# Optimization experiments

Hardware: AMD Instinct MI355X
Metric: run time of the kernel (lower is better)

Reference implementation:

```python
import jax, jax.numpy as jnp
import numpy as np

B, F, T, N, A, E_INC, NUM_EDGES, C_OUT = 32, 64, 20, 512, 64, 2048, 128, 128
C_IN = F + A


def setup_inputs() -> dict:
    key = jax.random.key(0)
    k = jax.random.split(key, 6)
    x = jax.random.normal(k[0], (B, F, T, N), dtype=jnp.float32)
    H = jax.random.randint(k[1], (B, T, 2, E_INC), 0, NUM_EDGES)  # row0: node ids, row1: hyperedge ids
    ssa = jax.random.normal(k[2], (B, T, N, A), dtype=jnp.float32)
    W = jax.random.uniform(k[3], (B, T, E_INC), dtype=jnp.float32)  # unused by conv (matches original)
    theta = jax.random.normal(k[4], (C_OUT, C_IN), dtype=jnp.float32) / np.sqrt(C_IN).astype(np.float32)
    bias = jnp.zeros((C_OUT,), dtype=jnp.float32)
    return {"x": x, "H": H, "ssa": ssa, "W": W, "theta": theta, "bias": bias}


def _hconv(feat, hidx, theta, bias):
    # One PyG HypergraphConv (no attention, unit hyperedge weights):
    #   out = D^{-1} H B^{-1} H^T (X Theta^T) + b
    # feat: [N, C_in], hidx: [2, E_inc]
    node_idx, edge_idx = hidx[0], hidx[1]
    xp = feat @ theta.T  # [N, C_out]
    ones = jnp.ones(node_idx.shape, dtype=xp.dtype)
    deg_n = jax.ops.segment_sum(ones, node_idx, num_segments=N)         # D
    deg_e = jax.ops.segment_sum(ones, edge_idx, num_segments=NUM_EDGES)  # B
    Dinv = jnp.where(deg_n > 0, 1.0 / deg_n, 0.0)
    Binv = jnp.where(deg_e > 0, 1.0 / deg_e, 0.0)
    # node -> hyperedge aggregation
    edge_feat = Binv[:, None] * jax.ops.segment_sum(xp[node_idx], edge_idx, num_segments=NUM_EDGES)
    # hyperedge -> node aggregation
    out = Dinv[:, None] * jax.ops.segment_sum(edge_feat[edge_idx], node_idx, num_segments=N)
    return out + bias


def reference(x, H, ssa, W, theta, bias):
    # x: [B, F, T, N] -> [B, T, N, F], concat scene attention -> [B, T, N, C_in]
    feat = jnp.concatenate([jnp.transpose(x, (0, 2, 3, 1)), ssa], axis=-1)
    conv = lambda f, h: _hconv(f, h, theta, bias)
    out = jax.vmap(jax.vmap(conv))(feat, H)  # [B, T, N, C_out]
    # Original does a raw .reshape(B, C_out, T, N) (NOT a permute) -- replicate exactly.
    return out.reshape(B, C_OUT, T, N)
```

## Files before the change

kernel.cpp:

```cpp
#include <hip/hip_runtime.h>
#include <cstdint>
#include <cstddef>

namespace {

constexpr int B_ = 32, F_ = 64, T_ = 20, N_ = 512, A_ = 64;
constexpr int EINC = 2048, NEDGE = 128, COUT = 128, CIN = 128;
constexpr int THREADS = 1024;

constexpr int L_SRT  = 0;
constexpr int L_ESRT = 2048;
constexpr int L_OFFN = 4096;
constexpr int L_OFFE = 4612;
constexpr int L_DEGN = 4744;
constexpr int L_DEGE = 5256;
constexpr int L_CURN = 5384;
constexpr int L_CURE = 5896;
constexpr int L_U    = 6024;
constexpr int L_ST   = 14472;
constexpr int LDS_WORDS = 19592;
constexpr int LDS_BYTES = LDS_WORDS * 4;
constexpr int XQ_STRIDE = 66;

typedef float f32x8 __attribute__((ext_vector_type(8)));
typedef float f32x4v __attribute__((ext_vector_type(4)));
typedef short bf16x8v __attribute__((ext_vector_type(8)));

__device__ inline unsigned short f2bf(float f) {
    unsigned int u = __float_as_uint(f);
    u = u + 0x7FFFu + ((u >> 16) & 1u);
    return (unsigned short)(u >> 16);
}
__device__ inline unsigned packbf(float lo, float hi) {
    return ((unsigned)f2bf(hi) << 16) | (unsigned)f2bf(lo);
}

#define LOAD_CHUNK(CC, DST) do {                                              \
    const int c_ = (CC);                                                      \
    if (c_ < 4) {                                                             \
        const float* xr_ = x + (((size_t)b * F_ + (c_ * 16 + hf * 8)) * T_ + t) * N_ + n; \
        _Pragma("unroll")                                                     \
        for (int j_ = 0; j_ < 8; ++j_)                                        \
            DST[j_] = xr_[(size_t)j_ * T_ * N_];                              \
    } else {                                                                  \
        const float* sr_ = ssa + ((size_t)bt * N_ + n) * A_ + (c_ - 4) * 16 + hf * 8; \
        float4 u0_ = *(const float4*)(sr_);                                   \
        float4 u1_ = *(const float4*)(sr_ + 4);                               \
        DST[0] = u0_.x; DST[1] = u0_.y; DST[2] = u0_.z; DST[3] = u0_.w;       \
        DST[4] = u1_.x; DST[5] = u1_.y; DST[6] = u1_.z; DST[7] = u1_.w;       \
    }                                                                         \
} while (0)

#define P6PASS(P) do {                                                        \
    const int lw_ = tid & 31;                                                 \
    const int g_  = tid >> 5;                                                 \
    float2 bsv_ = *(const float2*)(bias + (P) * 64 + 2 * lw_);                \
    for (int nn_ = g_; nn_ < N_; nn_ += 32) {                                 \
        int o0_ = s_ofn[nn_], o1_ = s_ofn[nn_ + 1];                           \
        float f0_ = 0.f, f1_ = 0.f;                                           \
        for (int k_ = o0_; k_ < o1_; ++k_) {                                  \
            int e_ = s_srt[k_];                                               \
            float2 xv_ = *(const float2*)(s_xq + e_ * XQ_STRIDE + 2 * lw_);   \
            f0_ += xv_.x; f1_ += xv_.y;                                       \
        }                                                                     \
        float dinv_ = (o1_ > o0_) ? 1.0f / (float)(o1_ - o0_) : 0.0f;         \
        size_t ob_ = ((size_t)bt * N_ + nn_) * COUT + (P) * 64 + 2 * lw_;     \
        *(float2*)(out + ob_) = make_float2(f0_ * dinv_ + bsv_.x,             \
                                            f1_ * dinv_ + bsv_.y);            \
    }                                                                         \
} while (0)

__global__ __launch_bounds__(256)
void theta_pack(const float* __restrict__ theta, unsigned* __restrict__ ws) {
    int w = blockIdx.x * 256 + threadIdx.x;
    int f = w >> 8, rem = w & 255;
    int l = rem >> 2, kq = rem & 3;
    int kk = f & 3, cti = (f >> 2) & 3, ch2 = f >> 4;
    int co = ch2 * 64 + cti * 16 + (l & 15);
    int ci = kk * 32 + (l >> 4) * 8 + kq * 2;
    const float2 tv = *(const float2*)(theta + (size_t)co * CIN + ci);
    ws[w] = packbf(tv.x, tv.y);
}

__global__ __launch_bounds__(THREADS, 8)
void hgconv(const float* __restrict__ x, const int* __restrict__ H,
            const float* __restrict__ ssa, const float* __restrict__ theta,
            const float* __restrict__ bias, float* __restrict__ out,
            const unsigned* __restrict__ thw)
{
    extern __shared__ float sf[];
    int* si = (int*)sf;

    const int tid = (int)threadIdx.x;
    const int bt  = (int)blockIdx.x;
    const int b   = bt / T_;
    const int t   = bt - b * T_;

    int* s_srt = si + L_SRT;
    int* s_esr = si + L_ESRT;
    int* s_ofn = si + L_OFFN;
    int* s_ofe = si + L_OFFE;
    int* s_dgn = si + L_DEGN;
    int* s_dge = si + L_DEGE;
    int* s_cun = si + L_CURN;
    int* s_cue = si + L_CURE;
    int* s_nid = si + L_U;
    int* s_eid = si + L_U + EINC;
    unsigned* s_eq16 = (unsigned*)si + L_U;
    float* s_xq = sf + L_U;
    unsigned* s_st16 = (unsigned*)si + L_ST;

    const int n  = tid & (N_ - 1);
    const int hf = tid >> 9;

    const int* Hb = H + (size_t)bt * (2 * EINC);
    #pragma unroll
    for (int k = 0; k < EINC / THREADS; ++k) {
        int i = tid + k * THREADS;
        s_nid[i] = Hb[i];
        s_eid[i] = Hb[EINC + i];
    }
    if (tid < N_)    s_dgn[tid] = 0;
    if (tid < NEDGE) s_dge[tid] = 0;
    __syncthreads();

    #pragma unroll
    for (int k = 0; k < EINC / THREADS; ++k) {
        int i = tid + k * THREADS;
        atomicAdd(&s_dgn[s_nid[i]], 1);
        atomicAdd(&s_dge[s_eid[i]], 1);
    }
    __syncthreads();

    const bool act = s_dgn[n] > 0;
    f32x8 vv;
    if (act) LOAD_CHUNK(0, vv);

    if (tid < 64) {
        const int l = tid;
        int d0 = s_dge[2 * l], d1 = s_dge[2 * l + 1];
        int run = d0 + d1;
        int scan = run;
        #pragma unroll
        for (int d = 1; d < 64; d <<= 1) {
            int o = __shfl_up(scan, d);
            if (l >= d) scan += o;
        }
        int excl = scan - run;
        s_ofe[2 * l] = excl;
        s_ofe[2 * l + 1] = excl + d0;
        if (l == 63) s_ofe[NEDGE] = scan;
    } else if (tid < 128) {
        const int l = tid & 63;
        int v, loc[8], run = 0;
        #pragma unroll
        for (int q = 0; q < 8; ++q) { v = s_dgn[l * 8 + q]; loc[q] = run; run += v; }
        int scan = run;
        #pragma unroll
        for (int d = 1; d < 64; d <<= 1) {
            int o = __shfl_up(scan, d);
            if (l >= d) scan += o;
        }
        int excl = scan - run;
        #pragma unroll
        for (int q = 0; q < 8; ++q) s_ofn[l * 8 + q] = excl + loc[q];
        if (l == 63) s_ofn[N_] = scan;
    }
    __syncthreads();

    if (tid < N_)    s_cun[tid] = s_ofn[tid];
    if (tid < NEDGE) s_cue[tid] = s_ofe[tid];
    __syncthreads();

    #pragma unroll
    for (int k = 0; k < EINC / THREADS; ++k) {
        int i = tid + k * THREADS;
        int nd = s_nid[i];
        int e  = s_eid[i];
        int pe = atomicAdd(&s_cue[e], 1);
        s_esr[pe] = nd;
        int pn = atomicAdd(&s_cun[nd], 1);
        s_srt[pn] = e;
    }
    __syncthreads();

    const int eg = tid >> 3;
    const int ep = tid & 7;
    for (int c = 0; c < 8; ++c) {
        if (act) {
            unsigned w0 = packbf(vv[0], vv[1]), w1 = packbf(vv[2], vv[3]);
            unsigned w2 = packbf(vv[4], vv[5]), w3 = packbf(vv[6], vv[7]);
            unsigned* sp = s_st16 + n * 10 + hf * 4;
            *(uint2*)(sp)     = make_uint2(w0, w1);
            *(uint2*)(sp + 2) = make_uint2(w2, w3);
        }
        __syncthreads();

        f32x8 nv;
        if (c < 7 && act) LOAD_CHUNK(c + 1, nv);

        {
            int k0 = s_ofe[eg], k1 = s_ofe[eg + 1];
            float a0 = 0.f, a1 = 0.f;
            int k = k0;
            for (; k + 1 < k1; k += 2) {
                unsigned pA = s_st16[s_esr[k] * 10 + ep];
                unsigned pB = s_st16[s_esr[k + 1] * 10 + ep];
                a0 += __uint_as_float(pA << 16) + __uint_as_float(pB << 16);
                a1 += __uint_as_float(pA & 0xFFFF0000u) + __uint_as_float(pB & 0xFFFF0000u);
            }
            if (k < k1) {
                unsigned pA = s_st16[s_esr[k] * 10 + ep];
                a0 += __uint_as_float(pA << 16);
                a1 += __uint_as_float(pA & 0xFFFF0000u);
            }
            float binv = (k1 > k0) ? 1.0f / (float)(k1 - k0) : 0.0f;
            int p = c * 8 + ep;
            s_eq16[eg * 64 + (p ^ ((eg & 7) << 2))] = packbf(a0 * binv, a1 * binv);
        }
        __syncthreads();

        if (c < 7 && act) vv = nv;
    }

    {
        const int wv = tid >> 6, l = tid & 63;
        const int rt = wv >> 1, ch2 = wv & 1;
        const int r  = rt * 16 + (l & 15);
        const int q  = l >> 4;
        const int lco = l & 15;

        bf16x8v av[4];
        #pragma unroll
        for (int kk = 0; kk < 4; ++kk) {
            int aw = r * 64 + ((kk * 16 + q * 4) ^ ((r & 7) << 2));
            av[kk] = *(const bf16x8v*)(s_eq16 + aw);
        }
        f32x4v acc[4];
        #pragma unroll
        for (int i = 0; i < 4; ++i) acc[i] = (f32x4v){0.f, 0.f, 0.f, 0.f};

        if (thw) {
            #pragma unroll
            for (int cti = 0; cti < 4; ++cti) {
                #pragma unroll
                for (int kk = 0; kk < 4; ++kk) {
                    int f = (ch2 * 4 + cti) * 4 + kk;
                    uint4 u = *((const uint4*)thw + f * 64 + l);
                    bf16x8v bv = *(const bf16x8v*)&u;
                    acc[cti] = __builtin_amdgcn_mfma_f32_16x16x32_bf16(av[kk], bv, acc[cti], 0, 0, 0);
                }
            }
        } else {
            #pragma unroll
            for (int cti = 0; cti < 4; ++cti) {
                const int co = ch2 * 64 + cti * 16 + lco;
                #pragma unroll
                for (int kk = 0; kk < 4; ++kk) {
                    const float* tp = theta + (size_t)co * CIN + kk * 32 + q * 8;
                    float4 t0 = *(const float4*)tp;
                    float4 t1 = *(const float4*)(tp + 4);
                    unsigned pw[4] = { packbf(t0.x, t0.y), packbf(t0.z, t0.w),
                                       packbf(t1.x, t1.y), packbf(t1.z, t1.w) };
                    bf16x8v bv = *(const bf16x8v*)pw;
                    acc[cti] = __builtin_amdgcn_mfma_f32_16x16x32_bf16(av[kk], bv, acc[cti], 0, 0, 0);
                }
            }
        }
        __syncthreads();

        if (ch2 == 0) {
            #pragma unroll
            for (int cti = 0; cti < 4; ++cti)
                #pragma unroll
                for (int reg = 0; reg < 4; ++reg)
                    s_xq[(rt * 16 + q * 4 + reg) * XQ_STRIDE + cti * 16 + lco] = acc[cti][reg];
        }
        __syncthreads();
        P6PASS(0);
        __syncthreads();
        if (ch2 == 1) {
            #pragma unroll
            for (int cti = 0; cti < 4; ++cti)
                #pragma unroll
                for (int reg = 0; reg < 4; ++reg)
                    s_xq[(rt * 16 + q * 4 + reg) * XQ_STRIDE + cti * 16 + lco] = acc[cti][reg];
        }
        __syncthreads();
        P6PASS(1);
    }
}

}

extern "C" void kernel_launch(void* const* d_in, const int* in_sizes, int n_in,
                              void* d_out, int out_size, void* d_ws, size_t ws_size,
                              hipStream_t stream) {
    const float* x     = (const float*)d_in[0];
    const int*   H     = (const int*)d_in[1];
    const float* ssa   = (const float*)d_in[2];
    const float* theta = (const float*)d_in[4];
    const float* bias  = (const float*)d_in[5];
    float* outp = (float*)d_out;

    const bool use_ws = (d_ws != nullptr) && (ws_size >= 32768);
    if (use_ws)
        hipLaunchKernelGGL(theta_pack, dim3(32), dim3(256), 0, stream,
                           theta, (unsigned*)d_ws);

    (void)hipFuncSetAttribute((const void*)&hgconv,
                              hipFuncAttributeMaxDynamicSharedMemorySize, LDS_BYTES);

    hipLaunchKernelGGL(hgconv, dim3(B_ * T_), dim3(THREADS), LDS_BYTES, stream,
                       x, H, ssa, theta, bias, outp,
                       use_ws ? (const unsigned*)d_ws : nullptr);
}
```

Before: 91.95 us.

## Halve block size, compact LDS indices, interleave MFMA with edge aggregation

The block shrinks from 1024 to 512 threads, each handling one node and 16 channels per chunk. Sorted index arrays are stored as bytes and shorts instead of ints, and a XOR swizzle replaces the padded LDS layout. This cuts LDS use from about 78KB to about 38KB so more blocks can be resident per CU. The theta GEMM is now issued incrementally: after every two channel chunks, each wave runs MFMAs for one K-slice across all 8 output tiles, keeping 8 accumulators live. The cost is higher register pressure and more per-thread gather work in the aggregation loops.

```diff
diff --git a/kernel.cpp b/kernel.cpp
--- a/kernel.cpp
+++ b/kernel.cpp
@@ -6,23 +6,22 @@
 
 constexpr int B_ = 32, F_ = 64, T_ = 20, N_ = 512, A_ = 64;
 constexpr int EINC = 2048, NEDGE = 128, COUT = 128, CIN = 128;
-constexpr int THREADS = 1024;
-
-constexpr int L_SRT  = 0;
-constexpr int L_ESRT = 2048;
-constexpr int L_OFFN = 4096;
-constexpr int L_OFFE = 4612;
-constexpr int L_DEGN = 4744;
-constexpr int L_DEGE = 5256;
-constexpr int L_CURN = 5384;
-constexpr int L_CURE = 5896;
-constexpr int L_U    = 6024;
-constexpr int L_ST   = 14472;
-constexpr int LDS_WORDS = 19592;
+constexpr int THREADS = 512;
+
+constexpr int L_SRT8 = 0;
+constexpr int L_OFN  = 512;
+constexpr int L_OFE  = 1028;
+constexpr int L_DGE  = 1160;
+constexpr int L_CUE  = 1288;
+constexpr int L_DGN  = 1416;
+constexpr int L_CUN  = 1928;
+constexpr int L_ESR  = 2440;
+constexpr int L_EQ   = 3464;
+constexpr int L_ST   = 5512;
+constexpr int LDS_WORDS = 9608;
 constexpr int LDS_BYTES = LDS_WORDS * 4;
-constexpr int XQ_STRIDE = 66;
-
-typedef float f32x8 __attribute__((ext_vector_type(8)));
+
+typedef unsigned u32x8 __attribute__((ext_vector_type(8)));
 typedef float f32x4v __attribute__((ext_vector_type(4)));
 typedef short bf16x8v __attribute__((ext_vector_type(8)));
 
@@ -34,33 +33,40 @@
 __device__ inline unsigned packbf(float lo, float hi) {
     return ((unsigned)f2bf(hi) << 16) | (unsigned)f2bf(lo);
 }
+__device__ inline float bflo(unsigned p) { return __uint_as_float(p << 16); }
+__device__ inline float bfhi(unsigned p) { return __uint_as_float(p & 0xFFFF0000u); }
 
 #define LOAD_CHUNK(CC, DST) do {                                              \
     const int c_ = (CC);                                                      \
     if (c_ < 4) {                                                             \
-        const float* xr_ = x + (((size_t)b * F_ + (c_ * 16 + hf * 8)) * T_ + t) * N_ + n; \
+        const float* xr_ = x + (((size_t)b * F_ + c_ * 16) * T_ + t) * N_ + n; \
         _Pragma("unroll")                                                     \
-        for (int j_ = 0; j_ < 8; ++j_)                                        \
-            DST[j_] = xr_[(size_t)j_ * T_ * N_];                              \
+        for (int m_ = 0; m_ < 8; ++m_) {                                      \
+            float f0_ = xr_[(size_t)(2 * m_) * (T_ * N_)];                    \
+            float f1_ = xr_[(size_t)(2 * m_ + 1) * (T_ * N_)];                \
+            DST[m_] = packbf(f0_, f1_);                                       \
+        }                                                                     \
     } else {                                                                  \
-        const float* sr_ = ssa + ((size_t)bt * N_ + n) * A_ + (c_ - 4) * 16 + hf * 8; \
-        float4 u0_ = *(const float4*)(sr_);                                   \
-        float4 u1_ = *(const float4*)(sr_ + 4);                               \
-        DST[0] = u0_.x; DST[1] = u0_.y; DST[2] = u0_.z; DST[3] = u0_.w;       \
-        DST[4] = u1_.x; DST[5] = u1_.y; DST[6] = u1_.z; DST[7] = u1_.w;       \
+        const float* sr_ = ssa + ((size_t)bt * N_ + n) * A_ + (c_ - 4) * 16;  \
+        _Pragma("unroll")                                                     \
+        for (int m_ = 0; m_ < 4; ++m_) {                                      \
+            float4 u_ = *(const float4*)(sr_ + 4 * m_);                       \
+            DST[2 * m_]     = packbf(u_.x, u_.y);                             \
+            DST[2 * m_ + 1] = packbf(u_.z, u_.w);                             \
+        }                                                                     \
     }                                                                         \
 } while (0)
 
 #define P6PASS(P) do {                                                        \
     const int lw_ = tid & 31;                                                 \
-    const int g_  = tid >> 5;                                                 \
+    const int g_  = tid >> 5;                                      \
     float2 bsv_ = *(const float2*)(bias + (P) * 64 + 2 * lw_);                \
-    for (int nn_ = g_; nn_ < N_; nn_ += 32) {                                 \
+    for (int nn_ = g_; nn_ < N_; nn_ += 16) {                                 \
         int o0_ = s_ofn[nn_], o1_ = s_ofn[nn_ + 1];                           \
         float f0_ = 0.f, f1_ = 0.f;                                           \
         for (int k_ = o0_; k_ < o1_; ++k_) {                                  \
-            int e_ = s_srt[k_];                                               \
-            float2 xv_ = *(const float2*)(s_xq + e_ * XQ_STRIDE + 2 * lw_);   \
+            int e_ = (int)s_srt8[k_];                                         \
+            float2 xv_ = *(const float2*)(s_xq + e_ * 64 + 2 * lw_);          \
             f0_ += xv_.x; f1_ += xv_.y;                                       \
         }                                                                     \
         float dinv_ = (o1_ > o0_) ? 1.0f / (float)(o1_ - o0_) : 0.0f;         \
@@ -75,8 +81,8 @@
     int w = blockIdx.x * 256 + threadIdx.x;
     int f = w >> 8, rem = w & 255;
     int l = rem >> 2, kq = rem & 3;
-    int kk = f & 3, cti = (f >> 2) & 3, ch2 = f >> 4;
-    int co = ch2 * 64 + cti * 16 + (l & 15);
+    int kk = f & 3, ct = f >> 2;
+    int co = ct * 16 + (l & 15);
     int ci = kk * 32 + (l >> 4) * 8 + kq * 2;
     const float2 tv = *(const float2*)(theta + (size_t)co * CIN + ci);
     ws[w] = packbf(tv.x, tv.y);
@@ -96,22 +102,21 @@
     const int b   = bt / T_;
     const int t   = bt - b * T_;
 
-    int* s_srt = si + L_SRT;
-    int* s_esr = si + L_ESRT;
-    int* s_ofn = si + L_OFFN;
-    int* s_ofe = si + L_OFFE;
-    int* s_dgn = si + L_DEGN;
-    int* s_dge = si + L_DEGE;
-    int* s_cun = si + L_CURN;
-    int* s_cue = si + L_CURE;
-    int* s_nid = si + L_U;
-    int* s_eid = si + L_U + EINC;
-    unsigned* s_eq16 = (unsigned*)si + L_U;
-    float* s_xq = sf + L_U;
-    unsigned* s_st16 = (unsigned*)si + L_ST;
-
-    const int n  = tid & (N_ - 1);
-    const int hf = tid >> 9;
+    unsigned char*  s_srt8  = (unsigned char*)(si + L_SRT8);
+    int*            s_ofn   = si + L_OFN;
+    int*            s_ofe   = si + L_OFE;
+    int*            s_dge   = si + L_DGE;
+    int*            s_cue   = si + L_CUE;
+    int*            s_dgn   = si + L_DGN;
+    int*            s_cun   = si + L_CUN;
+    unsigned short* s_esr16 = (unsigned short*)(si + L_ESR);
+    unsigned*       s_eq16  = (unsigned*)(si + L_EQ);
+    unsigned*       s_st16  = (unsigned*)(si + L_ST);
+    int*            s_nid   = si + L_EQ;
+    int*            s_eid   = si + L_EQ + EINC;
+    float*          s_xq    = sf + L_DGN;
+
+    const int n = tid;
 
     const int* Hb = H + (size_t)bt * (2 * EINC);
     #pragma unroll
@@ -120,7 +125,7 @@
         s_nid[i] = Hb[i];
         s_eid[i] = Hb[EINC + i];
     }
-    if (tid < N_)    s_dgn[tid] = 0;
+    s_dgn[tid] = 0;
     if (tid < NEDGE) s_dge[tid] = 0;
     __syncthreads();
 
@@ -133,7 +138,7 @@
     __syncthreads();
 
     const bool act = s_dgn[n] > 0;
-    f32x8 vv;
+    u32x8 vv;
     if (act) LOAD_CHUNK(0, vv);
 
     if (tid < 64) {
@@ -168,7 +173,7 @@
     }
     __syncthreads();
 
-    if (tid < N_)    s_cun[tid] = s_ofn[tid];
+    s_cun[tid] = s_ofn[tid];
     if (tid < NEDGE) s_cue[tid] = s_ofe[tid];
     __syncthreads();
 
@@ -178,117 +183,97 @@
         int nd = s_nid[i];
         int e  = s_eid[i];
         int pe = atomicAdd(&s_cue[e], 1);
-        s_esr[pe] = nd;
+        s_esr16[pe] = (unsigned short)nd;
         int pn = atomicAdd(&s_cun[nd], 1);
-        s_srt[pn] = e;
-    }
-    __syncthreads();
-
-    const int eg = tid >> 3;
-    const int ep = tid & 7;
+        s_srt8[pn] = (unsigned char)e;
+    }
+    __syncthreads();
+
+    const int eg = tid >> 2;
+    const int ep = tid & 3;
+    const int wv = tid >> 6, l = tid & 63;
+    const int q  = l >> 4, lco = l & 15;
+    const int r  = wv * 16 + lco;
+    const int aoff = r * 16 + 4 * (q ^ (r & 3) ^ ((r >> 2) & 3));
+    const int k0 = s_ofe[eg], k1 = s_ofe[eg + 1];
+    const float binv = (k1 > k0) ? 1.0f / (float)(k1 - k0) : 0.0f;
+
+    f32x4v acc[8];
+    #pragma unroll
+    for (int i = 0; i < 8; ++i) acc[i] = (f32x4v){0.f, 0.f, 0.f, 0.f};
+
     for (int c = 0; c < 8; ++c) {
         if (act) {
-            unsigned w0 = packbf(vv[0], vv[1]), w1 = packbf(vv[2], vv[3]);
-            unsigned w2 = packbf(vv[4], vv[5]), w3 = packbf(vv[6], vv[7]);
-            unsigned* sp = s_st16 + n * 10 + hf * 4;
-            *(uint2*)(sp)     = make_uint2(w0, w1);
-            *(uint2*)(sp + 2) = make_uint2(w2, w3);
+            #pragma unroll
+            for (int p2 = 0; p2 < 4; ++p2) {
+                unsigned* sp = s_st16 + n * 8
+                             + 2 * (p2 ^ (n & 3) ^ ((n >> 2) & 3));
+                *(uint2*)sp = make_uint2(vv[2 * p2], vv[2 * p2 + 1]);
+            }
         }
         __syncthreads();
 
-        f32x8 nv;
+        u32x8 nv;
         if (c < 7 && act) LOAD_CHUNK(c + 1, nv);
 
         {
-            int k0 = s_ofe[eg], k1 = s_ofe[eg + 1];
-            float a0 = 0.f, a1 = 0.f;
-            int k = k0;
-            for (; k + 1 < k1; k += 2) {
-                unsigned pA = s_st16[s_esr[k] * 10 + ep];
-                unsigned pB = s_st16[s_esr[k + 1] * 10 + ep];
-                a0 += __uint_as_float(pA << 16) + __uint_as_float(pB << 16);
-                a1 += __uint_as_float(pA & 0xFFFF0000u) + __uint_as_float(pB & 0xFFFF0000u);
+            float a0 = 0.f, a1 = 0.f, a2 = 0.f, a3 = 0.f;
+            for (int k = k0; k < k1; ++k) {
+                int nd = (int)s_esr16[k];
+                uint2 pr = *(const uint2*)(s_st16 + nd * 8
+                                + 2 * (ep ^ (nd & 3) ^ ((nd >> 2) & 3)));
+                a0 += bflo(pr.x); a1 += bfhi(pr.x);
+                a2 += bflo(pr.y); a3 += bfhi(pr.y);
             }
-            if (k < k1) {
-                unsigned pA = s_st16[s_esr[k] * 10 + ep];
-                a0 += __uint_as_float(pA << 16);
-                a1 += __uint_as_float(pA & 0xFFFF0000u);
-            }
-            float binv = (k1 > k0) ? 1.0f / (float)(k1 - k0) : 0.0f;
-            int p = c * 8 + ep;
-            s_eq16[eg * 64 + (p ^ ((eg & 7) << 2))] = packbf(a0 * binv, a1 * binv);
+            int slot = (((c & 1) * 2 + (ep >> 1)) ^ (eg & 3) ^ ((eg >> 2) & 3));
+            *(uint2*)(s_eq16 + eg * 16 + 4 * slot + (ep & 1) * 2) =
+                make_uint2(packbf(a0 * binv, a1 * binv), packbf(a2 * binv, a3 * binv));
         }
         __syncthreads();
 
-        if (c < 7 && act) vv = nv;
-    }
-
-    {
-        const int wv = tid >> 6, l = tid & 63;
-        const int rt = wv >> 1, ch2 = wv & 1;
-        const int r  = rt * 16 + (l & 15);
-        const int q  = l >> 4;
-        const int lco = l & 15;
-
-        bf16x8v av[4];
-        #pragma unroll
-        for (int kk = 0; kk < 4; ++kk) {
-            int aw = r * 64 + ((kk * 16 + q * 4) ^ ((r & 7) << 2));
-            av[kk] = *(const bf16x8v*)(s_eq16 + aw);
-        }
-        f32x4v acc[4];
-        #pragma unroll
-        for (int i = 0; i < 4; ++i) acc[i] = (f32x4v){0.f, 0.f, 0.f, 0.f};
-
-        if (thw) {
-            #pragma unroll
-            for (int cti = 0; cti < 4; ++cti) {
+        if (c & 1) {
+            const int p = c >> 1;
+            bf16x8v av = *(const bf16x8v*)(s_eq16 + aoff);
+            if (thw) {
                 #pragma unroll
-                for (int kk = 0; kk < 4; ++kk) {
-                    int f = (ch2 * 4 + cti) * 4 + kk;
-                    uint4 u = *((const uint4*)thw + f * 64 + l);
-                    bf16x8v bv = *(const bf16x8v*)&u;
-                    acc[cti] = __builtin_amdgcn_mfma_f32_16x16x32_bf16(av[kk], bv, acc[cti], 0, 0, 0);
+                for (int ct = 0; ct < 8; ++ct) {
+                    uint4 u = ((const uint4*)thw)[(ct * 4 + p) * 64 + l];
+                    acc[ct] = __builtin_amdgcn_mfma_f32_16x16x32_bf16(
+                        av, *(const bf16x8v*)&u, acc[ct], 0, 0, 0);
                 }
-            }
-        } else {
-            #pragma unroll
-            for (int cti = 0; cti < 4; ++cti) {
-                const int co = ch2 * 64 + cti * 16 + lco;
+            } else {
                 #pragma unroll
-                for (int kk = 0; kk < 4; ++kk) {
-                    const float* tp = theta + (size_t)co * CIN + kk * 32 + q * 8;
+                for (int ct = 0; ct < 8; ++ct) {
+                    const float* tp = theta + (size_t)(ct * 16 + lco) * CIN
+                                    + p * 32 + q * 8;
                     float4 t0 = *(const float4*)tp;
                     float4 t1 = *(const float4*)(tp + 4);
                     unsigned pw[4] = { packbf(t0.x, t0.y), packbf(t0.z, t0.w),
                                        packbf(t1.x, t1.y), packbf(t1.z, t1.w) };
-                    bf16x8v bv = *(const bf16x8v*)pw;
-                    acc[cti] = __builtin_amdgcn_mfma_f32_16x16x32_bf16(av[kk], bv, acc[cti], 0, 0, 0);
+                    acc[ct] = __builtin_amdgcn_mfma_f32_16x16x32_bf16(
+                        av, *(const bf16x8v*)pw, acc[ct], 0, 0, 0);
                 }
             }
         }
-        __syncthreads();
-
-        if (ch2 == 0) {
-            #pragma unroll
-            for (int cti = 0; cti < 4; ++cti)
-                #pragma unroll
-                for (int reg = 0; reg < 4; ++reg)
-                    s_xq[(rt * 16 + q * 4 + reg) * XQ_STRIDE + cti * 16 + lco] = acc[cti][reg];
-        }
-        __syncthreads();
-        P6PASS(0);
-        __syncthreads();
-        if (ch2 == 1) {
-            #pragma unroll
-            for (int cti = 0; cti < 4; ++cti)
-                #pragma unroll
-                for (int reg = 0; reg < 4; ++reg)
-                    s_xq[(rt * 16 + q * 4 + reg) * XQ_STRIDE + cti * 16 + lco] = acc[cti][reg];
-        }
-        __syncthreads();
-        P6PASS(1);
-    }
+        if (c < 7 && act) vv = nv;
+    }
+    __syncthreads();
+
+    #pragma unroll
+    for (int c2 = 0; c2 < 4; ++c2)
+        #pragma unroll
+        for (int reg = 0; reg < 4; ++reg)
+            s_xq[(wv * 16 + q * 4 + reg) * 64 + c2 * 16 + lco] = acc[c2][reg];
+    __syncthreads();
+    P6PASS(0);
+    __syncthreads();
+    #pragma unroll
+    for (int c2 = 0; c2 < 4; ++c2)
+        #pragma unroll
+        for (int reg = 0; reg < 4; ++reg)
+            s_xq[(wv * 16 + q * 4 + reg) * 64 + c2 * 16 + lco] = acc[4 + c2][reg];
+    __syncthreads();
+    P6PASS(1);
 }
 
 }
@@ -308,9 +293,6 @@
         hipLaunchKernelGGL(theta_pack, dim3(32), dim3(256), 0, stream,
                            theta, (unsigned*)d_ws);
 
-    (void)hipFuncSetAttribute((const void*)&hgconv,
-                              hipFuncAttributeMaxDynamicSharedMemorySize, LDS_BYTES);
-
     hipLaunchKernelGGL(hgconv, dim3(B_ * T_), dim3(THREADS), LDS_BYTES, stream,
                        x, H, ssa, theta, bias, outp,
                        use_ws ? (const unsigned*)d_ws : nullptr);
```

After: 151.8 us. +65.1%, slower.
